# Kernel tuning notes

Measured on AMD Instinct MI355X. Metric: run time of the kernel, lower is better.

The kernel has to match this reference:

```python
import jax, jax.numpy as jnp
import numpy as np
import math

POOL_H = 8
POOL_W = 16
LATENT_H = 48
LATENT_W = 80
VISUAL_LEN = 7680   # 2 frames of 48*80 latent tokens
SPARSITY = 0.9
NUM_HEADS = 16
HEAD_DIM = 64


def _reorg_restore():
    # part/block/sub-block token reorganization so pooled sub-blocks are contiguous
    part = LATENT_W * POOL_H          # 640
    blk = LATENT_W                    # 80
    sub = POOL_W                      # 16
    bpp = part // blk                 # blocks per part = 8
    spb = blk // sub                  # sub-blocks per block = 5
    # orig index = b*blk + c*sub + i ; new order iterates (c, b, i)
    pat = np.arange(part).reshape(bpp, spb, sub).transpose(1, 0, 2).reshape(-1)
    nparts = VISUAL_LEN // part
    reorg = (np.arange(nparts)[:, None] * part + pat[None, :]).reshape(-1)
    restore = np.argsort(reorg)       # inverse permutation
    return jnp.asarray(reorg), jnp.asarray(restore)

REORG_IDX, RESTORE_IDX = _reorg_restore()


def _draft_attn_map(q, k):
    # q, k: [L, H, D] -> pooled attention map [H, S, S]
    L, H, D = q.shape
    nf = L // (LATENT_H * LATENT_W)
    def pool(x):
        # 2D avg-pool each frame (dims divide exactly -> reshape+mean)
        x = x.reshape(nf, LATENT_H // POOL_H, POOL_H, LATENT_W // POOL_W, POOL_W, H, D)
        return x.mean(axis=(2, 4)).reshape(-1, H, D)   # [S, H, D]
    qs, ks = pool(q), pool(k)
    scores = jnp.einsum('lhd,mhd->hlm', qs, ks) / math.sqrt(D)
    return jax.nn.softmax(scores, axis=-1)


def _percentile_mask(attn, r):
    # keep top-r fraction of entries per head: threshold = max of k smallest
    H, S, _ = attn.shape
    n = S * S
    kk = int((1.0 - r) * n)           # number of entries dropped (0 < kk < n here)
    thr = jnp.sort(attn.reshape(H, n), axis=-1)[:, kk - 1]
    return attn >= thr[:, None, None]


def _head_attn(qh, kh, vh, mblk):
    # qh/kh/vh: [L, D]; mblk: [nb, nb] bool block mask, block size L//nb (=128)
    L, D = qh.shape
    nb = mblk.shape[0]
    mB = L // nb
    s = (qh @ kh.T) * (1.0 / math.sqrt(D))              # [L, L]
    s = jnp.where(mblk[:, None, :, None], s.reshape(nb, mB, nb, mB), -jnp.inf)
    s = s.reshape(L, L)
    m = jnp.max(s, axis=-1, keepdims=True)
    m = jnp.where(jnp.isfinite(m), m, 0.0)              # fully-masked rows -> 0 output
    p = jnp.exp(s - m)                                  # exp(-inf) = 0
    p = p / jnp.maximum(p.sum(-1, keepdims=True), 1e-30)
    return p @ vh


def _forward(q, k, v, batch_size, max_seqlen_q):
    attn = _draft_attn_map(q, k)                        # [H, S, S]
    mask = _percentile_mask(attn, 1.0 - SPARSITY)       # [H, S, S] bool
    qr, kr, vr = q[REORG_IDX], k[REORG_IDX], v[REORG_IDX]
    qh = jnp.swapaxes(qr, 0, 1)                         # [H, L, D]
    kh = jnp.swapaxes(kr, 0, 1)
    vh = jnp.swapaxes(vr, 0, 1)
    f = jax.checkpoint(lambda t: _head_attn(*t))
    out = jax.lax.map(f, (qh, kh, vh, mask))            # sequential over heads: [H, L, D]
    x = jnp.swapaxes(out, 0, 1)[RESTORE_IDX]            # [L, H, D]
    return x.reshape(batch_size, max_seqlen_q, q.shape[1], q.shape[2])


def setup_inputs() -> dict:
    key = jax.random.key(0)
    kq, kk, kv = jax.random.split(key, 3)
    L = VISUAL_LEN
    q = jax.random.normal(kq, (L, NUM_HEADS, HEAD_DIM), dtype=jnp.float32)
    k = jax.random.normal(kk, (L, NUM_HEADS, HEAD_DIM), dtype=jnp.float32)
    v = jax.random.normal(kv, (L, NUM_HEADS, HEAD_DIM), dtype=jnp.float32)
    return {
        'q': q, 'k': k, 'v': v,
        'cu_seqlens_q': jnp.array([0, L], dtype=jnp.int32),
        'cu_seqlens_kv': jnp.array([0, L], dtype=jnp.int32),
        'max_seqlen_q': L,
        'max_seqlen_kv': L,
        'batch_size': 1,
    }


def reference(q, k, v, cu_seqlens_q, cu_seqlens_kv, max_seqlen_q, max_seqlen_kv, batch_size):
    return _forward(q, k, v, batch_size, max_seqlen_q)
```

## Files before the change

kernel.cpp:

```cpp
#include <hip/hip_runtime.h>

#define L_TOK   7680
#define NHEAD   16
#define HDIM    64
#define NBLK    60
#define KEEP    361
#define QS_OFF   0u
#define KS_OFF   491520u
#define CNT_OFF  983040u
#define COL_OFF  986880u
#define KHM_OFF  1217280u
#define VTM_OFF  16945920u
#define ORD_OFF  32674560u

typedef short bf16x8 __attribute__((ext_vector_type(8)));
typedef short bf16x4 __attribute__((ext_vector_type(4)));
typedef float f32x4  __attribute__((ext_vector_type(4)));

__device__ __forceinline__ unsigned int cvtpk(float lo, float hi) {
  unsigned int r;
  asm("v_cvt_pk_bf16_f32 %0, %1, %2" : "=v"(r) : "v"(lo), "v"(hi));
  return r;
}

__device__ __forceinline__ f32x4 mfma16(bf16x4 a, bf16x4 b, f32x4 c) {
#if __has_builtin(__builtin_amdgcn_mfma_f32_16x16x16bf16_1k)
  return __builtin_amdgcn_mfma_f32_16x16x16bf16_1k(a, b, c, 0, 0, 0);
#else
  asm("v_mfma_f32_16x16x16_bf16 %0, %1, %2, %0" : "+v"(c) : "v"(a), "v"(b));
  return c;
#endif
}

__device__ __forceinline__ void gll16(const unsigned short* gsrc, unsigned short* ldst) {
  __builtin_amdgcn_global_load_lds(
      (const __attribute__((address_space(1))) unsigned int*)gsrc,
      (__attribute__((address_space(3))) unsigned int*)ldst, 16, 0, 0);
}

__global__ __launch_bounds__(256) void prep_kernel(
    const float* __restrict__ qin, const float* __restrict__ kin,
    const float* __restrict__ vin, double* __restrict__ qs, double* __restrict__ ks,
    unsigned short* __restrict__ khm, unsigned short* __restrict__ vtm) {
  __shared__ float stg[128 * 68];
  __shared__ double psum[4][64];
  const int h = blockIdx.x, blk = blockIdx.y, t = threadIdx.x;
  const int p = blk / 5, c = blk % 5;
  const int q4 = t >> 6, dq = t & 63;

  unsigned short* kdst = khm + (size_t)(h * 60 + blk) * 8192;
  #pragma unroll
  for (int it = 0; it < 4; ++it) {
    int sidx = it * 256 + t;  int row = sidx >> 3, s = sidx & 7;
    int tok = p * 640 + (row >> 4) * 80 + c * 16 + (row & 15);
    const float* src = kin + (size_t)tok * 1024 + h * 64 + s * 8;
    float4 a = ((const float4*)src)[0], b = ((const float4*)src)[1];
    uint4 un; un.x = cvtpk(a.x, a.y); un.y = cvtpk(a.z, a.w);
    un.z = cvtpk(b.x, b.y); un.w = cvtpk(b.z, b.w);
    *(uint4*)(kdst + row * 64 + ((s ^ (row & 7)) * 8)) = un;
    *(float4*)&stg[row * 68 + s * 8] = a;
    *(float4*)&stg[row * 68 + s * 8 + 4] = b;
  }
  __syncthreads();
  { double acc = 0.0;
    for (int r = 0; r < 32; ++r) acc += (double)stg[(q4 * 32 + r) * 68 + dq];
    psum[q4][dq] = acc; }
  __syncthreads();
  if (t < 64)
    ks[(size_t)(h * 60 + blk) * 64 + t] =
        (psum[0][t] + psum[1][t] + psum[2][t] + psum[3][t]) * (1.0 / 128.0);
  __syncthreads();

  #pragma unroll
  for (int it = 0; it < 4; ++it) {
    int sidx = it * 256 + t;  int row = sidx >> 3, s = sidx & 7;
    int tok = p * 640 + (row >> 4) * 80 + c * 16 + (row & 15);
    const float* src = qin + (size_t)tok * 1024 + h * 64 + s * 8;
    float4 a = ((const float4*)src)[0], b = ((const float4*)src)[1];
    *(float4*)&stg[row * 68 + s * 8] = a;
    *(float4*)&stg[row * 68 + s * 8 + 4] = b;
  }
  __syncthreads();
  { double acc = 0.0;
    for (int r = 0; r < 32; ++r) acc += (double)stg[(q4 * 32 + r) * 68 + dq];
    psum[q4][dq] = acc; }
  __syncthreads();
  if (t < 64)
    qs[(size_t)(h * 60 + blk) * 64 + t] =
        (psum[0][t] + psum[1][t] + psum[2][t] + psum[3][t]) * (1.0 / 128.0);
  __syncthreads();

  #pragma unroll
  for (int it = 0; it < 8; ++it) {
    int idx = it * 256 + t;  int row = idx >> 4, f4 = idx & 15;
    int tok = p * 640 + (row >> 4) * 80 + c * 16 + (row & 15);
    float4 a = ((const float4*)(vin + (size_t)tok * 1024 + h * 64))[f4];
    *(float4*)&stg[row * 68 + f4 * 4] = a;
  }
  __syncthreads();
  unsigned short* vdst = vtm + (size_t)(h * 60 + blk) * 8192;
  #pragma unroll
  for (int it = 0; it < 4; ++it) {
    int u = it * 256 + t;  int d = u >> 4, sl = u & 15;
    int kbase = (sl >> 2) * 32 + (sl & 3) * 4;
    uint4 un;
    un.x = cvtpk(stg[(kbase + 0) * 68 + d],  stg[(kbase + 1) * 68 + d]);
    un.y = cvtpk(stg[(kbase + 2) * 68 + d],  stg[(kbase + 3) * 68 + d]);
    un.z = cvtpk(stg[(kbase + 16) * 68 + d], stg[(kbase + 17) * 68 + d]);
    un.w = cvtpk(stg[(kbase + 18) * 68 + d], stg[(kbase + 19) * 68 + d]);
    *(uint4*)(vdst + d * 128 + ((sl ^ (d & 7)) * 8)) = un;
  }
}

__global__ void scores_kernel(const double* __restrict__ qs, const double* __restrict__ ks,
                              float* __restrict__ probsF) {
  const int i = blockIdx.x, h = blockIdx.y, j = threadIdx.x;
  const double* qr = qs + (size_t)(h * 60 + i) * 64;
  double sc = -1.0e300;
  if (j < 60) {
    const double* kr = ks + (size_t)(h * 60 + j) * 64;
    double a0 = 0, a1 = 0, a2 = 0, a3 = 0;
    #pragma unroll
    for (int d = 0; d < 64; d += 4) {
      a0 += qr[d]     * kr[d];
      a1 += qr[d + 1] * kr[d + 1];
      a2 += qr[d + 2] * kr[d + 2];
      a3 += qr[d + 3] * kr[d + 3];
    }
    sc = ((a0 + a1) + (a2 + a3)) * 0.125;
  }
  double m = sc;
  #pragma unroll
  for (int o = 32; o; o >>= 1) m = fmax(m, __shfl_xor(m, o, 64));
  double e = (j < 60) ? exp(sc - m) : 0.0;
  double ssum = e;
  #pragma unroll
  for (int o = 32; o; o >>= 1) ssum += __shfl_xor(ssum, o, 64);
  if (j < 60) probsF[(size_t)(h * 60 + i) * 60 + j] = (float)(e / ssum);
}

__global__ __launch_bounds__(256) void select_kernel(const float* __restrict__ probsF,
                                                     int* __restrict__ counts,
                                                     int* __restrict__ cols,
                                                     int* __restrict__ order) {
  const int h = blockIdx.x, t = threadIdx.x;
  __shared__ float pb[3600];
  __shared__ int hist[2048];
  __shared__ int warr[4];
  __shared__ int sh_digit, sh_above;
  __shared__ int scnt[60];

  unsigned int myv[15];
  #pragma unroll
  for (int m2 = 0; m2 < 15; ++m2) {
    int i = t + m2 * 256;
    float v = 0.0f;
    if (i < 3600) { v = probsF[(size_t)h * 3600 + i]; pb[i] = v; }
    myv[m2] = __float_as_uint(v);
  }
  __syncthreads();

  unsigned int prefix = 0;
  int rank = KEEP;
  const int lane = t & 63, w = t >> 6;
  #pragma unroll
  for (int pass = 0; pass < 3; ++pass) {
    const int shift = (pass == 0) ? 21 : (pass == 1) ? 10 : 0;
    const int width = (pass == 2) ? 10 : 11;
    const int dmask = (1 << width) - 1;
    for (int i = t; i < 2048; i += 256) hist[i] = 0;
    __syncthreads();
    const int hb = shift + width;
    #pragma unroll
    for (int m2 = 0; m2 < 15; ++m2) {
      unsigned int u = myv[m2];
      if (u && (pass == 0 || (u >> hb) == (prefix >> hb)))
        atomicAdd(&hist[(int)((u >> shift) & dmask)], 1);
    }
    __syncthreads();
    const int base = t * 8;
    int bcnt[8], s = 0;
    #pragma unroll
    for (int b = 0; b < 8; ++b) { bcnt[b] = hist[base + b]; s += bcnt[b]; }
    int incl = s;
    #pragma unroll
    for (int o = 1; o < 64; o <<= 1) {
      int y = __shfl_down(incl, o, 64);
      if (lane + o < 64) incl += y;
    }
    if (lane == 0) warr[w] = incl;
    __syncthreads();
    int above_w = 0;
    for (int w2 = w + 1; w2 < 4; ++w2) above_w += warr[w2];
    int run = (incl - s) + above_w;
    #pragma unroll
    for (int b = 7; b >= 0; --b) {
      int c = bcnt[b];
      if (c > 0 && run < rank && run + c >= rank) { sh_digit = base + b; sh_above = run; }
      run += c;
    }
    __syncthreads();
    prefix |= ((unsigned int)sh_digit) << shift;
    rank -= sh_above;
    __syncthreads();
  }

  const float thr = __uint_as_float(prefix);
  if (t < 60) {
    int cnt = 0;
    int tmp[60];
    for (int j = 0; j < 60; ++j)
      if (pb[t * 60 + j] >= thr) tmp[cnt++] = j;
    for (int j = 0; j < cnt; ++j) cols[(size_t)(h * 60 + t) * 60 + j] = tmp[j];
    counts[h * 60 + t] = cnt;
    scnt[t] = cnt;
  }
  __syncthreads();
  if (t < 60) {
    int c = scnt[t], rk = 0;
    for (int j = 0; j < 60; ++j) {
      int cj = scnt[j];
      rk += (cj > c) || (cj == c && j < t);
    }
    order[h * 60 + rk] = t;
  }
}

__global__ __launch_bounds__(256, 2) void attn_kernel(
    const float* __restrict__ qin, const unsigned short* __restrict__ khm,
    const unsigned short* __restrict__ vtm, const int* __restrict__ counts,
    const int* __restrict__ cols, const int* __restrict__ order,
    float* __restrict__ out) {
  const int h = blockIdx.x;
  const int qb = order[h * 60 + blockIdx.y];
  const int t = threadIdx.x, w = t >> 6, lane = t & 63;
  const int g = lane >> 4, n = lane & 15, sw = n & 7;
  __shared__ __align__(16) unsigned short LDSb[32768];
  #define KT(b) (LDSb + (b) * 8192)
  #define VT(b) (LDSb + 16384 + (b) * 8192)

  const int cnt = counts[h * 60 + qb];
  const int pq = qb / 5, cq = qb % 5;
  if (cnt == 0) {
    for (int i = t; i < 2048; i += 256) {
      int row = i >> 4, f4 = i & 15;
      int tok = pq * 640 + (row >> 4) * 80 + cq * 16 + (row & 15);
      float4 z = {0.f, 0.f, 0.f, 0.f};
      *(float4*)(out + (size_t)tok * 1024 + h * 64 + f4 * 4) = z;
    }
    return;
  }

  const int* mycols = cols + (size_t)(h * 60 + qb) * 60;
  int colv = mycols[lane < cnt ? lane : 0];

  bf16x8 aq[2][2];
  #pragma unroll
  for (int qt = 0; qt < 2; ++qt) {
    int lq = w * 32 + qt * 16 + n;
    int tok = pq * 640 + (lq >> 4) * 80 + cq * 16 + (lq & 15);
    const float* qrow = qin + (size_t)tok * 1024 + h * 64;
    #pragma unroll
    for (int hh = 0; hh < 2; ++hh) {
      const float4* s4 = (const float4*)(qrow + hh * 32 + g * 8);
      float4 a = s4[0], b2 = s4[1];
      union { bf16x8 v; unsigned int uw[4]; } un;
      un.uw[0] = cvtpk(a.x, a.y);  un.uw[1] = cvtpk(a.z, a.w);
      un.uw[2] = cvtpk(b2.x, b2.y); un.uw[3] = cvtpk(b2.z, b2.w);
      aq[qt][hh] = un.v;
    }
  }

  const f32x4 zero4 = {0.f, 0.f, 0.f, 0.f};
  f32x4 acco[2][4];
  float mst[2] = {-1.0e38f, -1.0e38f}, lst[2] = {0.f, 0.f};
  #pragma unroll
  for (int qt = 0; qt < 2; ++qt)
    #pragma unroll
    for (int dt = 0; dt < 4; ++dt) acco[qt][dt] = zero4;

  const unsigned short* khm_h = khm + (size_t)(h * 60) * 8192;
  const unsigned short* vtm_h = vtm + (size_t)(h * 60) * 8192;
  const float C2 = 0.18033688011112042f;

  {
    int kb0 = __shfl(colv, 0, 64);
    asm volatile("s_waitcnt vmcnt(0)" ::: "memory");
    const unsigned short* ksrc = khm_h + (size_t)kb0 * 8192;
    const unsigned short* vsrc = vtm_h + (size_t)kb0 * 8192;
    #pragma unroll
    for (int j = 0; j < 4; ++j) {
      gll16(ksrc + (size_t)((w * 4 + j) * 512) + lane * 8, KT(0) + (w * 4 + j) * 512);
      gll16(vsrc + (size_t)((w * 4 + j) * 512) + lane * 8, VT(0) + (w * 4 + j) * 512);
    }
  }

  for (int ki = 0; ki < cnt; ++ki) {
    const int b = ki & 1;
    if (ki + 1 < cnt) {
      int kbn = __shfl(colv, ki + 1, 64);
      const unsigned short* ksrc = khm_h + (size_t)kbn * 8192;
      const unsigned short* vsrc = vtm_h + (size_t)kbn * 8192;
      #pragma unroll
      for (int j = 0; j < 4; ++j) {
        gll16(ksrc + (size_t)((w * 4 + j) * 512) + lane * 8, KT(b ^ 1) + (w * 4 + j) * 512);
        gll16(vsrc + (size_t)((w * 4 + j) * 512) + lane * 8, VT(b ^ 1) + (w * 4 + j) * 512);
      }
      asm volatile("s_waitcnt vmcnt(8)" ::: "memory");
    } else {
      asm volatile("s_waitcnt vmcnt(0)" ::: "memory");
    }
    __syncthreads();

    f32x4 accs[2][8];
    #pragma unroll
    for (int qt = 0; qt < 2; ++qt)
      #pragma unroll
      for (int kt = 0; kt < 8; ++kt) accs[qt][kt] = zero4;
    __builtin_amdgcn_s_setprio(1);
    #pragma unroll
    for (int kt = 0; kt < 8; ++kt) {
      int rowbase = (kt * 16 + n) * 64;
      bf16x8 k0 = *(const bf16x8*)&KT(b)[rowbase + ((g ^ sw) * 8)];
      bf16x8 k1 = *(const bf16x8*)&KT(b)[rowbase + (((4 + g) ^ sw) * 8)];
      accs[0][kt] = __builtin_amdgcn_mfma_f32_16x16x32_bf16(k0, aq[0][0], accs[0][kt], 0, 0, 0);
      accs[0][kt] = __builtin_amdgcn_mfma_f32_16x16x32_bf16(k1, aq[0][1], accs[0][kt], 0, 0, 0);
      accs[1][kt] = __builtin_amdgcn_mfma_f32_16x16x32_bf16(k0, aq[1][0], accs[1][kt], 0, 0, 0);
      accs[1][kt] = __builtin_amdgcn_mfma_f32_16x16x32_bf16(k1, aq[1][1], accs[1][kt], 0, 0, 0);
    }
    __builtin_amdgcn_s_setprio(0);

    bf16x4 pbv[2][8];
    #pragma unroll
    for (int qt = 0; qt < 2; ++qt) {
      float mloc = -1.0e38f;
      #pragma unroll
      for (int kt = 0; kt < 8; ++kt) {
        float m01 = fmaxf(fmaxf(accs[qt][kt][0], accs[qt][kt][1]),
                          fmaxf(accs[qt][kt][2], accs[qt][kt][3]));
        mloc = fmaxf(mloc, m01);
      }
      mloc = fmaxf(mloc, __shfl_xor(mloc, 16, 64));
      mloc = fmaxf(mloc, __shfl_xor(mloc, 32, 64));
      float mn = fmaxf(mst[qt], mloc * C2);
      float fsq = __builtin_amdgcn_exp2f(mst[qt] - mn);
      mst[qt] = mn;
      float rs0 = 0.f, rs1 = 0.f, rs2 = 0.f, rs3 = 0.f;
      #pragma unroll
      for (int kt = 0; kt < 8; ++kt) {
        float p0 = __builtin_amdgcn_exp2f(fmaf(accs[qt][kt][0], C2, -mn));
        float p1 = __builtin_amdgcn_exp2f(fmaf(accs[qt][kt][1], C2, -mn));
        float p2 = __builtin_amdgcn_exp2f(fmaf(accs[qt][kt][2], C2, -mn));
        float p3 = __builtin_amdgcn_exp2f(fmaf(accs[qt][kt][3], C2, -mn));
        rs0 += p0; rs1 += p1; rs2 += p2; rs3 += p3;
        union { unsigned int u[2]; bf16x4 v; } pb;
        pb.u[0] = cvtpk(p0, p1);
        pb.u[1] = cvtpk(p2, p3);
        pbv[qt][kt] = pb.v;
      }
      float rsum = (rs0 + rs1) + (rs2 + rs3);
      rsum += __shfl_xor(rsum, 16, 64);
      rsum += __shfl_xor(rsum, 32, 64);
      lst[qt] = lst[qt] * fsq + rsum;
      #pragma unroll
      for (int dt = 0; dt < 4; ++dt)
        #pragma unroll
        for (int r = 0; r < 4; ++r) acco[qt][dt][r] *= fsq;
    }

    __builtin_amdgcn_s_setprio(1);
    #pragma unroll
    for (int kp = 0; kp < 4; ++kp) {
      #pragma unroll
      for (int dt = 0; dt < 4; ++dt) {
        int d = dt * 16 + n;
        bf16x8 vv = *(const bf16x8*)&VT(b)[d * 128 + (((kp * 4 + g) ^ sw) * 8)];
        bf16x4 vlo = __builtin_shufflevector(vv, vv, 0, 1, 2, 3);
        bf16x4 vhi = __builtin_shufflevector(vv, vv, 4, 5, 6, 7);
        acco[0][dt] = mfma16(vlo, pbv[0][2 * kp],     acco[0][dt]);
        acco[0][dt] = mfma16(vhi, pbv[0][2 * kp + 1], acco[0][dt]);
        acco[1][dt] = mfma16(vlo, pbv[1][2 * kp],     acco[1][dt]);
        acco[1][dt] = mfma16(vhi, pbv[1][2 * kp + 1], acco[1][dt]);
      }
    }
    __builtin_amdgcn_s_setprio(0);
    __syncthreads();
  }

  float* Ot = (float*)LDSb;
  #pragma unroll
  for (int qt = 0; qt < 2; ++qt) {
    float inv = 1.0f / lst[qt];
    int q = w * 32 + qt * 16 + n;
    #pragma unroll
    for (int dt = 0; dt < 4; ++dt)
      #pragma unroll
      for (int r = 0; r < 4; ++r)
        Ot[q * 68 + dt * 16 + 4 * g + r] = acco[qt][dt][r] * inv;
  }
  __syncthreads();
  for (int i = t; i < 2048; i += 256) {
    int q = i >> 4, f4 = i & 15;
    int tok = pq * 640 + (q >> 4) * 80 + cq * 16 + (q & 15);
    float4 val = *(float4*)&Ot[q * 68 + f4 * 4];
    *(float4*)(out + (size_t)tok * 1024 + h * 64 + f4 * 4) = val;
  }
  #undef KT
  #undef VT
}

extern "C" void kernel_launch(void* const* d_in, const int* in_sizes, int n_in,
                              void* d_out, int out_size, void* d_ws, size_t ws_size,
                              hipStream_t stream) {
  const float* qin = (const float*)d_in[0];
  const float* kin = (const float*)d_in[1];
  const float* vin = (const float*)d_in[2];
  char* ws = (char*)d_ws;
  double* qs = (double*)(ws + QS_OFF);
  double* ks = (double*)(ws + KS_OFF);
  int* counts = (int*)(ws + CNT_OFF);
  int* cols = (int*)(ws + COL_OFF);
  float* probsF = (float*)(ws + COL_OFF);
  unsigned short* khm = (unsigned short*)(ws + KHM_OFF);
  unsigned short* vtm = (unsigned short*)(ws + VTM_OFF);
  int* order = (int*)(ws + ORD_OFF);
  float* outp = (float*)d_out;

  prep_kernel<<<dim3(16, 60), 256, 0, stream>>>(qin, kin, vin, qs, ks, khm, vtm);
  scores_kernel<<<dim3(60, 16), 64, 0, stream>>>(qs, ks, probsF);
  select_kernel<<<16, 256, 0, stream>>>(probsF, counts, cols, order);
  attn_kernel<<<dim3(16, 60), 256, 0, stream>>>(qin, khm, vtm, counts, cols, order, outp);
}
```

Measured before the change: 96.28 us.

## Stream half-tiles of K/V to cut LDS and raise attention occupancy

The attention kernel now processes each 128-key block as two 64-key halves, halving the K/V double-buffer LDS footprint so launch bounds can request 4 blocks per SM instead of 2. The V-transposed layout in the prep kernel is reorganised into two contiguous 64-key halves to match. The softmax scale is folded into Q at bf16 conversion, removing a multiply per score. The Q pooling pass now reads Q straight from global memory into registers instead of staging through LDS, dropping some barriers. The trade-offs are twice as many loop iterations and barriers per key block, and slightly different rounding because Q is scaled before the bf16 conversion.

```diff
diff --git a/kernel.cpp b/kernel.cpp
--- a/kernel.cpp
+++ b/kernel.cpp
@@ -62,33 +62,13 @@
     *(float4*)&stg[row * 68 + s * 8 + 4] = b;
   }
   __syncthreads();
-  { double acc = 0.0;
-    for (int r = 0; r < 32; ++r) acc += (double)stg[(q4 * 32 + r) * 68 + dq];
-    psum[q4][dq] = acc; }
+  { double ka = 0.0;
+    for (int r = 0; r < 32; ++r) ka += (double)stg[(q4 * 32 + r) * 68 + dq];
+    psum[q4][dq] = ka; }
   __syncthreads();
   if (t < 64)
     ks[(size_t)(h * 60 + blk) * 64 + t] =
         (psum[0][t] + psum[1][t] + psum[2][t] + psum[3][t]) * (1.0 / 128.0);
-  __syncthreads();
-
-  #pragma unroll
-  for (int it = 0; it < 4; ++it) {
-    int sidx = it * 256 + t;  int row = sidx >> 3, s = sidx & 7;
-    int tok = p * 640 + (row >> 4) * 80 + c * 16 + (row & 15);
-    const float* src = qin + (size_t)tok * 1024 + h * 64 + s * 8;
-    float4 a = ((const float4*)src)[0], b = ((const float4*)src)[1];
-    *(float4*)&stg[row * 68 + s * 8] = a;
-    *(float4*)&stg[row * 68 + s * 8 + 4] = b;
-  }
-  __syncthreads();
-  { double acc = 0.0;
-    for (int r = 0; r < 32; ++r) acc += (double)stg[(q4 * 32 + r) * 68 + dq];
-    psum[q4][dq] = acc; }
-  __syncthreads();
-  if (t < 64)
-    qs[(size_t)(h * 60 + blk) * 64 + t] =
-        (psum[0][t] + psum[1][t] + psum[2][t] + psum[3][t]) * (1.0 / 128.0);
-  __syncthreads();
 
   #pragma unroll
   for (int it = 0; it < 8; ++it) {
@@ -97,18 +77,37 @@
     float4 a = ((const float4*)(vin + (size_t)tok * 1024 + h * 64))[f4];
     *(float4*)&stg[row * 68 + f4 * 4] = a;
   }
-  __syncthreads();
+  double a0 = 0, a1 = 0, a2 = 0, a3 = 0;
+  #pragma unroll
+  for (int i = 0; i < 32; i += 4) {
+    #pragma unroll
+    for (int j2 = 0; j2 < 4; ++j2) {
+      int row = q4 * 32 + i + j2;
+      int tok = p * 640 + (row >> 4) * 80 + c * 16 + (row & 15);
+      double v = (double)qin[(size_t)tok * 1024 + h * 64 + dq];
+      if (j2 == 0) a0 += v; else if (j2 == 1) a1 += v;
+      else if (j2 == 2) a2 += v; else a3 += v;
+    }
+  }
+  __syncthreads();
+  psum[q4][dq] = (a0 + a1) + (a2 + a3);
+  __syncthreads();
+  if (t < 64)
+    qs[(size_t)(h * 60 + blk) * 64 + t] =
+        (psum[0][t] + psum[1][t] + psum[2][t] + psum[3][t]) * (1.0 / 128.0);
+
   unsigned short* vdst = vtm + (size_t)(h * 60 + blk) * 8192;
   #pragma unroll
   for (int it = 0; it < 4; ++it) {
     int u = it * 256 + t;  int d = u >> 4, sl = u & 15;
-    int kbase = (sl >> 2) * 32 + (sl & 3) * 4;
+    int half = sl >> 3, slot = sl & 7;
+    int kbase = half * 64 + (slot >> 2) * 32 + (slot & 3) * 4;
     uint4 un;
     un.x = cvtpk(stg[(kbase + 0) * 68 + d],  stg[(kbase + 1) * 68 + d]);
     un.y = cvtpk(stg[(kbase + 2) * 68 + d],  stg[(kbase + 3) * 68 + d]);
     un.z = cvtpk(stg[(kbase + 16) * 68 + d], stg[(kbase + 17) * 68 + d]);
     un.w = cvtpk(stg[(kbase + 18) * 68 + d], stg[(kbase + 19) * 68 + d]);
-    *(uint4*)(vdst + d * 128 + ((sl ^ (d & 7)) * 8)) = un;
+    *(uint4*)(vdst + half * 4096 + d * 64 + ((slot ^ (d & 7)) * 8)) = un;
   }
 }
 
@@ -226,7 +225,7 @@
   }
 }
 
-__global__ __launch_bounds__(256, 2) void attn_kernel(
+__global__ __launch_bounds__(256, 4) void attn_kernel(
     const float* __restrict__ qin, const unsigned short* __restrict__ khm,
     const unsigned short* __restrict__ vtm, const int* __restrict__ counts,
     const int* __restrict__ cols, const int* __restrict__ order,
@@ -235,9 +234,10 @@
   const int qb = order[h * 60 + blockIdx.y];
   const int t = threadIdx.x, w = t >> 6, lane = t & 63;
   const int g = lane >> 4, n = lane & 15, sw = n & 7;
-  __shared__ __align__(16) unsigned short LDSb[32768];
-  #define KT(b) (LDSb + (b) * 8192)
-  #define VT(b) (LDSb + 16384 + (b) * 8192)
+  __shared__ __align__(16) float LDSf[128 * 68];
+  unsigned short* LDSb = (unsigned short*)LDSf;
+  #define KT(b) (LDSb + (b) * 4096)
+  #define VT(b) (LDSb + 8192 + (b) * 4096)
 
   const int cnt = counts[h * 60 + qb];
   const int pq = qb / 5, cq = qb % 5;
@@ -254,6 +254,7 @@
   const int* mycols = cols + (size_t)(h * 60 + qb) * 60;
   int colv = mycols[lane < cnt ? lane : 0];
 
+  const float C2 = 0.18033688011112042f;
   bf16x8 aq[2][2];
   #pragma unroll
   for (int qt = 0; qt < 2; ++qt) {
@@ -265,8 +266,8 @@
       const float4* s4 = (const float4*)(qrow + hh * 32 + g * 8);
       float4 a = s4[0], b2 = s4[1];
       union { bf16x8 v; unsigned int uw[4]; } un;
-      un.uw[0] = cvtpk(a.x, a.y);  un.uw[1] = cvtpk(a.z, a.w);
-      un.uw[2] = cvtpk(b2.x, b2.y); un.uw[3] = cvtpk(b2.z, b2.w);
+      un.uw[0] = cvtpk(a.x * C2, a.y * C2);   un.uw[1] = cvtpk(a.z * C2, a.w * C2);
+      un.uw[2] = cvtpk(b2.x * C2, b2.y * C2); un.uw[3] = cvtpk(b2.z * C2, b2.w * C2);
       aq[qt][hh] = un.v;
     }
   }
@@ -281,7 +282,7 @@
 
   const unsigned short* khm_h = khm + (size_t)(h * 60) * 8192;
   const unsigned short* vtm_h = vtm + (size_t)(h * 60) * 8192;
-  const float C2 = 0.18033688011112042f;
+  const int nht = cnt * 2;
 
   {
     int kb0 = __shfl(colv, 0, 64);
@@ -289,37 +290,38 @@
     const unsigned short* ksrc = khm_h + (size_t)kb0 * 8192;
     const unsigned short* vsrc = vtm_h + (size_t)kb0 * 8192;
     #pragma unroll
-    for (int j = 0; j < 4; ++j) {
-      gll16(ksrc + (size_t)((w * 4 + j) * 512) + lane * 8, KT(0) + (w * 4 + j) * 512);
-      gll16(vsrc + (size_t)((w * 4 + j) * 512) + lane * 8, VT(0) + (w * 4 + j) * 512);
-    }
-  }
-
-  for (int ki = 0; ki < cnt; ++ki) {
-    const int b = ki & 1;
-    if (ki + 1 < cnt) {
-      int kbn = __shfl(colv, ki + 1, 64);
-      const unsigned short* ksrc = khm_h + (size_t)kbn * 8192;
-      const unsigned short* vsrc = vtm_h + (size_t)kbn * 8192;
-      #pragma unroll
-      for (int j = 0; j < 4; ++j) {
-        gll16(ksrc + (size_t)((w * 4 + j) * 512) + lane * 8, KT(b ^ 1) + (w * 4 + j) * 512);
-        gll16(vsrc + (size_t)((w * 4 + j) * 512) + lane * 8, VT(b ^ 1) + (w * 4 + j) * 512);
+    for (int j = 0; j < 2; ++j) {
+      gll16(ksrc + (size_t)((w * 2 + j) * 512) + lane * 8, KT(0) + (w * 2 + j) * 512);
+      gll16(vsrc + (size_t)((w * 2 + j) * 512) + lane * 8, VT(0) + (w * 2 + j) * 512);
+    }
+  }
+
+  for (int ht = 0; ht < nht; ++ht) {
+    const int b = ht & 1;
+    if (ht + 1 < nht) {
+      int kbn = __shfl(colv, (ht + 1) >> 1, 64);
+      int hof = ((ht + 1) & 1) * 4096;
+      const unsigned short* ksrc = khm_h + (size_t)kbn * 8192 + hof;
+      const unsigned short* vsrc = vtm_h + (size_t)kbn * 8192 + hof;
+      #pragma unroll
+      for (int j = 0; j < 2; ++j) {
+        gll16(ksrc + (size_t)((w * 2 + j) * 512) + lane * 8, KT(b ^ 1) + (w * 2 + j) * 512);
+        gll16(vsrc + (size_t)((w * 2 + j) * 512) + lane * 8, VT(b ^ 1) + (w * 2 + j) * 512);
       }
-      asm volatile("s_waitcnt vmcnt(8)" ::: "memory");
+      asm volatile("s_waitcnt vmcnt(4)" ::: "memory");
     } else {
       asm volatile("s_waitcnt vmcnt(0)" ::: "memory");
     }
     __syncthreads();
 
-    f32x4 accs[2][8];
+    f32x4 accs[2][4];
     #pragma unroll
     for (int qt = 0; qt < 2; ++qt)
       #pragma unroll
-      for (int kt = 0; kt < 8; ++kt) accs[qt][kt] = zero4;
+      for (int kt = 0; kt < 4; ++kt) accs[qt][kt] = zero4;
     __builtin_amdgcn_s_setprio(1);
     #pragma unroll
-    for (int kt = 0; kt < 8; ++kt) {
+    for (int kt = 0; kt < 4; ++kt) {
       int rowbase = (kt * 16 + n) * 64;
       bf16x8 k0 = *(const bf16x8*)&KT(b)[rowbase + ((g ^ sw) * 8)];
       bf16x8 k1 = *(const bf16x8*)&KT(b)[rowbase + (((4 + g) ^ sw) * 8)];
@@ -330,28 +332,28 @@
     }
     __builtin_amdgcn_s_setprio(0);
 
-    bf16x4 pbv[2][8];
+    bf16x4 pbv[2][4];
     #pragma unroll
     for (int qt = 0; qt < 2; ++qt) {
       float mloc = -1.0e38f;
       #pragma unroll
-      for (int kt = 0; kt < 8; ++kt) {
+      for (int kt = 0; kt < 4; ++kt) {
         float m01 = fmaxf(fmaxf(accs[qt][kt][0], accs[qt][kt][1]),
                           fmaxf(accs[qt][kt][2], accs[qt][kt][3]));
         mloc = fmaxf(mloc, m01);
       }
       mloc = fmaxf(mloc, __shfl_xor(mloc, 16, 64));
       mloc = fmaxf(mloc, __shfl_xor(mloc, 32, 64));
-      float mn = fmaxf(mst[qt], mloc * C2);
+      float mn = fmaxf(mst[qt], mloc);
       float fsq = __builtin_amdgcn_exp2f(mst[qt] - mn);
       mst[qt] = mn;
       float rs0 = 0.f, rs1 = 0.f, rs2 = 0.f, rs3 = 0.f;
       #pragma unroll
-      for (int kt = 0; kt < 8; ++kt) {
-        float p0 = __builtin_amdgcn_exp2f(fmaf(accs[qt][kt][0], C2, -mn));
-        float p1 = __builtin_amdgcn_exp2f(fmaf(accs[qt][kt][1], C2, -mn));
-        float p2 = __builtin_amdgcn_exp2f(fmaf(accs[qt][kt][2], C2, -mn));
-        float p3 = __builtin_amdgcn_exp2f(fmaf(accs[qt][kt][3], C2, -mn));
+      for (int kt = 0; kt < 4; ++kt) {
+        float p0 = __builtin_amdgcn_exp2f(accs[qt][kt][0] - mn);
+        float p1 = __builtin_amdgcn_exp2f(accs[qt][kt][1] - mn);
+        float p2 = __builtin_amdgcn_exp2f(accs[qt][kt][2] - mn);
+        float p3 = __builtin_amdgcn_exp2f(accs[qt][kt][3] - mn);
         rs0 += p0; rs1 += p1; rs2 += p2; rs3 += p3;
         union { unsigned int u[2]; bf16x4 v; } pb;
         pb.u[0] = cvtpk(p0, p1);
@@ -370,11 +372,11 @@
 
     __builtin_amdgcn_s_setprio(1);
     #pragma unroll
-    for (int kp = 0; kp < 4; ++kp) {
+    for (int kp = 0; kp < 2; ++kp) {
       #pragma unroll
       for (int dt = 0; dt < 4; ++dt) {
         int d = dt * 16 + n;
-        bf16x8 vv = *(const bf16x8*)&VT(b)[d * 128 + (((kp * 4 + g) ^ sw) * 8)];
+        bf16x8 vv = *(const bf16x8*)&VT(b)[d * 64 + (((kp * 4 + g) ^ sw) * 8)];
         bf16x4 vlo = __builtin_shufflevector(vv, vv, 0, 1, 2, 3);
         bf16x4 vhi = __builtin_shufflevector(vv, vv, 4, 5, 6, 7);
         acco[0][dt] = mfma16(vlo, pbv[0][2 * kp],     acco[0][dt]);
@@ -387,7 +389,6 @@
     __syncthreads();
   }
 
-  float* Ot = (float*)LDSb;
   #pragma unroll
   for (int qt = 0; qt < 2; ++qt) {
     float inv = 1.0f / lst[qt];
@@ -396,13 +397,13 @@
     for (int dt = 0; dt < 4; ++dt)
       #pragma unroll
       for (int r = 0; r < 4; ++r)
-        Ot[q * 68 + dt * 16 + 4 * g + r] = acco[qt][dt][r] * inv;
+        LDSf[q * 68 + dt * 16 + 4 * g + r] = acco[qt][dt][r] * inv;
   }
   __syncthreads();
   for (int i = t; i < 2048; i += 256) {
     int q = i >> 4, f4 = i & 15;
     int tok = pq * 640 + (q >> 4) * 80 + cq * 16 + (q & 15);
-    float4 val = *(float4*)&Ot[q * 68 + f4 * 4];
+    float4 val = *(float4*)&LDSf[q * 68 + f4 * 4];
     *(float4*)(out + (size_t)tok * 1024 + h * 64 + f4 * 4) = val;
   }
   #undef KT
```

Measured after the change: 94.70 us. Within noise of the previous version (-1.6%).
